# Kernel optimization log

Measured on AMD Instinct MI355X. Metric: run time of the kernel, lower is better.

## Reference

```python
import jax, jax.numpy as jnp
import numpy as np
from jax import lax

BOS = 0
B, T, U = 8, 256, 64
IN, ENC_H, DEC_H, P, J, V = 80, 512, 512, 512, 512, 1024


def lstm_layer(x, Wih, Whh, b):
    """PyTorch-style LSTM layer. x: [B,T,I]; Wih: [4H,I]; Whh: [4H,H]; b: [4H]."""
    Bn = x.shape[0]
    H = Whh.shape[1]
    xp = jnp.einsum('bti,gi->btg', x, Wih) + b  # precompute input projections [B,T,4H]
    h0 = jnp.zeros((Bn, H), x.dtype)

    def step(carry, xt):
        h, c = carry
        g = xt + h @ Whh.T
        i, f, gg, o = jnp.split(g, 4, axis=-1)
        c = jax.nn.sigmoid(f) * c + jax.nn.sigmoid(i) * jnp.tanh(gg)
        h = jax.nn.sigmoid(o) * jnp.tanh(c)
        return (h, c), h

    _, hs = lax.scan(step, (h0, h0), xp.transpose(1, 0, 2))
    return hs.transpose(1, 0, 2)  # [B,T,H]


def setup_inputs() -> dict:
    key = jax.random.key(0)
    ks = jax.random.split(key, 20)
    s = 0.04  # ~1/sqrt(H) init scale
    inp = {
        'xs': jax.random.normal(ks[0], (B, T, IN), jnp.float32),
        'ys': jax.random.randint(ks[1], (B, U), 0, V),
        # encoder LSTM layer 0 / 1
        'enc_Wih0': jax.random.normal(ks[2], (4 * ENC_H, IN), jnp.float32) * s,
        'enc_Whh0': jax.random.normal(ks[3], (4 * ENC_H, ENC_H), jnp.float32) * s,
        'enc_b0': jnp.zeros((4 * ENC_H,), jnp.float32),
        'enc_Wih1': jax.random.normal(ks[4], (4 * ENC_H, ENC_H), jnp.float32) * s,
        'enc_Whh1': jax.random.normal(ks[5], (4 * ENC_H, ENC_H), jnp.float32) * s,
        'enc_b1': jnp.zeros((4 * ENC_H,), jnp.float32),
        'enc_projW': jax.random.normal(ks[6], (P, ENC_H), jnp.float32) * s,
        'enc_projb': jnp.zeros((P,), jnp.float32),
        # decoder
        'embed': jax.random.normal(ks[7], (V, DEC_H), jnp.float32) * s,
        'dec_Wih': jax.random.normal(ks[8], (4 * DEC_H, DEC_H), jnp.float32) * s,
        'dec_Whh': jax.random.normal(ks[9], (4 * DEC_H, DEC_H), jnp.float32) * s,
        'dec_b': jnp.zeros((4 * DEC_H,), jnp.float32),
        'dec_projW': jax.random.normal(ks[10], (P, DEC_H), jnp.float32) * s,
        'dec_projb': jnp.zeros((P,), jnp.float32),
        # joint MLP: Linear(2P -> J), Tanh, Linear(J -> V)
        'jW1': jax.random.normal(ks[11], (J, 2 * P), jnp.float32) * s,
        'jb1': jnp.zeros((J,), jnp.float32),
        'jW2': jax.random.normal(ks[12], (V, J), jnp.float32) * s,
        'jb2': jnp.zeros((V,), jnp.float32),
    }
    return inp


def reference(xs, ys, enc_Wih0, enc_Whh0, enc_b0, enc_Wih1, enc_Whh1, enc_b1,
              enc_projW, enc_projb, embed, dec_Wih, dec_Whh, dec_b,
              dec_projW, dec_projb, jW1, jb1, jW2, jb2):
    # Encoder: 2-layer LSTM + projection
    h = lstm_layer(xs, enc_Wih0, enc_Whh0, enc_b0)
    h = lstm_layer(h, enc_Wih1, enc_Whh1, enc_b1)
    h_enc = h @ enc_projW.T + enc_projb  # [B,T,P]

    # Decoder: BOS pad, embed, 1-layer LSTM + projection
    ys_p = jnp.pad(ys, ((0, 0), (1, 0)), constant_values=BOS)  # [B,U+1]
    e = embed[ys_p]
    hd = lstm_layer(e, dec_Wih, dec_Whh, dec_b)
    h_dec = hd @ dec_projW.T + dec_projb  # [B,U+1,P]

    # Joint: cat([h_enc,h_dec]) @ W1.T == h_enc @ W1[:,:P].T + h_dec @ W1[:,P:].T
    pre_enc = jnp.einsum('btp,jp->btj', h_enc, jW1[:, :P])
    pre_dec = jnp.einsum('bup,jp->buj', h_dec, jW1[:, P:])
    z = jnp.tanh(pre_enc[:, :, None, :] + pre_dec[:, None, :, :] + jb1)  # [B,T,U+1,J]
    logits = jnp.einsum('btuj,vj->btuv', z, jW2) + jb2  # [B,T,U+1,V]
    return logits
```

## Files before the change

kernel.cpp:

```cpp
#include <hip/hip_runtime.h>


typedef _Float16 f16;
typedef _Float16 f16x8 __attribute__((ext_vector_type(8)));
typedef float f32x4 __attribute__((ext_vector_type(4)));
using u32 = unsigned int;

#define BB   8
#define TT   256
#define UU1  65
#define HH   512
#define G4   2048
#define PP   512
#define JJ   512
#define VV   1024
#define SENT 0xFFFFFFFFu

#define LOADX(p)     __hip_atomic_load((p), __ATOMIC_RELAXED, __HIP_MEMORY_SCOPE_AGENT)
#define STOREX(p, v) __hip_atomic_store((p), (v), __ATOMIC_RELAXED, __HIP_MEMORY_SCOPE_AGENT)

static __device__ __forceinline__ u32 packf16(float a, float b) {
  f16 ha = (f16)a, hb = (f16)b;
  unsigned short ua = __builtin_bit_cast(unsigned short, ha);
  unsigned short ub = __builtin_bit_cast(unsigned short, hb);
  return (u32)ua | ((u32)ub << 16);
}
static __device__ __forceinline__ float sigm(float x) {
  x = fminf(30.f, fmaxf(-30.f, x));
  return __builtin_amdgcn_rcpf(1.f + __expf(-x));
}
static __device__ __forceinline__ float ftanh(float x) {
  x = fminf(15.f, fmaxf(-15.f, x));
  float t = __expf(2.f * x);
  return (t - 1.f) * __builtin_amdgcn_rcpf(t + 1.f);
}

__global__ void k_init(u32* __restrict__ p, int n, int z1, int z2) {
  int i = blockIdx.x * 256 + threadIdx.x;
  if (i >= n) return;
  bool z = (i < 2048) | ((u32)(i - z1) < 2048u) | ((u32)(i - z2) < 2048u);
  p[i] = z ? 0u : SENT;
}

struct CastSeg { const float* s; f16* d; int n4; };
struct CastArgs { CastSeg seg[10]; };
__global__ void k_cast_all(CastArgs a, int total4) {
  int i = blockIdx.x * 256 + threadIdx.x;
  if (i >= total4) return;
  int k = 0, off = i;
  while (off >= a.seg[k].n4) { off -= a.seg[k].n4; ++k; }
  const float4 v = *(const float4*)(a.seg[k].s + (size_t)off * 4);
  uint2 p; p.x = packf16(v.x, v.y); p.y = packf16(v.z, v.w);
  *(uint2*)(a.seg[k].d + (size_t)off * 4) = p;
}

__global__ void k_embed(const int* __restrict__ ys, const float* __restrict__ emb,
                        float* __restrict__ e) {
  int row = blockIdx.x;
  int b = row / UU1, u = row % UU1;
  int idx = (u == 0) ? 0 : ys[b * (UU1 - 1) + (u - 1)];
  const float4* s = (const float4*)(emb + (size_t)idx * HH);
  float4* d = (float4*)(e + (size_t)row * HH);
  d[threadIdx.x] = s[threadIdx.x];
}

__global__ void k_biasdot(const float* __restrict__ jW1, const float* __restrict__ encPb,
                          const float* __restrict__ dPb, const float* __restrict__ jb1,
                          float* __restrict__ bce, float* __restrict__ bcd) {
  int j = blockIdx.x * 256 + threadIdx.x;
  if (j >= 512) return;
  const float* rowE = jW1 + (size_t)j * 1024;
  const float* rowD = rowE + 512;
  float s1 = 0.f, s2 = 0.f;
  for (int p = 0; p < 512; p += 4) {
    float4 a = *(const float4*)(rowE + p), b = *(const float4*)(encPb + p);
    s1 += a.x * b.x + a.y * b.y + a.z * b.z + a.w * b.w;
    float4 c = *(const float4*)(rowD + p), d = *(const float4*)(dPb + p);
    s2 += c.x * d.x + c.y * d.y + c.z * d.z + c.w * d.w;
  }
  bce[j] = s1; bcd[j] = s2 + jb1[j];
}

__global__ __launch_bounds__(256) void k_gemm(
    const float* __restrict__ A, const f16* __restrict__ B,
    const float* __restrict__ bias, float* __restrict__ C,
    int M, int N, int K, int lda, int ldb) {
  __shared__ f16 As[128][72];
  __shared__ f16 Bs[128][72];
  int tid = threadIdx.x;
  int mb = blockIdx.y * 128, nb = blockIdx.x * 128;
  int wave = tid >> 6, lane = tid & 63;
  int wm = wave >> 1, wn = wave & 1;
  int rowa = lane & 15, kg = lane >> 4;
  f32x4 acc[4][4] = {};
  for (int k0 = 0; k0 < K; k0 += 64) {
    for (int idx = tid; idx < 2048; idx += 256) {
      int r = idx >> 4, cq = idx & 15;
      int gm = mb + r, gk = k0 + cq * 4;
      float4 v = make_float4(0.f, 0.f, 0.f, 0.f);
      if (gm < M && gk + 3 < K) v = *(const float4*)(A + (size_t)gm * lda + gk);
      uint2 p; p.x = packf16(v.x, v.y); p.y = packf16(v.z, v.w);
      *(uint2*)&As[r][cq * 4] = p;
    }
    for (int idx = tid; idx < 1024; idx += 256) {
      int r = idx >> 3, c8 = idx & 7;
      int gn = nb + r, gk = k0 + c8 * 8;
      uint4 v = make_uint4(0u, 0u, 0u, 0u);
      if (gn < N && gk + 7 < K) v = *(const uint4*)(B + (size_t)gn * ldb + gk);
      *(uint4*)&Bs[r][c8 * 8] = v;
    }
    __syncthreads();
#pragma unroll
    for (int kf = 0; kf < 2; ++kf) {
      f16x8 af[4], bf[4];
#pragma unroll
      for (int mt = 0; mt < 4; ++mt)
        af[mt] = *(const f16x8*)&As[wm * 64 + mt * 16 + rowa][kf * 32 + kg * 8];
#pragma unroll
      for (int nt = 0; nt < 4; ++nt)
        bf[nt] = *(const f16x8*)&Bs[wn * 64 + nt * 16 + rowa][kf * 32 + kg * 8];
#pragma unroll
      for (int mt = 0; mt < 4; ++mt)
#pragma unroll
        for (int nt = 0; nt < 4; ++nt)
          acc[mt][nt] = __builtin_amdgcn_mfma_f32_16x16x32_f16(af[mt], bf[nt], acc[mt][nt], 0, 0, 0);
    }
    __syncthreads();
  }
#pragma unroll
  for (int nt = 0; nt < 4; ++nt) {
    int gn = nb + wn * 64 + nt * 16 + rowa;
    float bv = bias ? bias[gn] : 0.f;
#pragma unroll
    for (int mt = 0; mt < 4; ++mt)
#pragma unroll
      for (int r = 0; r < 4; ++r) {
        int gm = mb + wm * 64 + mt * 16 + kg * 4 + r;
        if (gm < M) C[(size_t)gm * N + gn] = acc[mt][nt][r] + bv;
      }
  }
}

__global__ __launch_bounds__(256) void k_gemmT(
    const float* __restrict__ A, int lda, const f16* __restrict__ B2,
    f16* __restrict__ C16) {
  __shared__ f16 As[128][72];
  __shared__ f16 Bs[128][72];
  int tid = threadIdx.x;
  int mb = blockIdx.y * 128, nb = blockIdx.x * 128;
  int wave = tid >> 6, lane = tid & 63;
  int wm = wave >> 1, wn = wave & 1;
  int rowa = lane & 15, kg = lane >> 4;
  f32x4 acc[4][4] = {};
  for (int k0 = 0; k0 < 512; k0 += 64) {
    for (int idx = tid; idx < 2048; idx += 256) {
      int r = idx >> 4, cq = idx & 15;
      float4 v = *(const float4*)(A + (size_t)(mb + r) * lda + k0 + cq * 4);
      uint2 p; p.x = packf16(v.x, v.y); p.y = packf16(v.z, v.w);
      *(uint2*)&As[r][cq * 4] = p;
    }
    for (int idx = tid; idx < 1024; idx += 256) {
      int r = idx >> 4, c8 = idx & 15;
      uint4 v = *(const uint4*)(B2 + (size_t)(k0 + r) * 512 + nb + c8 * 8);
      f16 tmp[8]; *(uint4*)tmp = v;
#pragma unroll
      for (int e = 0; e < 8; ++e) Bs[c8 * 8 + e][r] = tmp[e];
    }
    __syncthreads();
#pragma unroll
    for (int kf = 0; kf < 2; ++kf) {
      f16x8 af[4], bf[4];
#pragma unroll
      for (int mt = 0; mt < 4; ++mt)
        af[mt] = *(const f16x8*)&As[wm * 64 + mt * 16 + rowa][kf * 32 + kg * 8];
#pragma unroll
      for (int nt = 0; nt < 4; ++nt)
        bf[nt] = *(const f16x8*)&Bs[wn * 64 + nt * 16 + rowa][kf * 32 + kg * 8];
#pragma unroll
      for (int mt = 0; mt < 4; ++mt)
#pragma unroll
        for (int nt = 0; nt < 4; ++nt)
          acc[mt][nt] = __builtin_amdgcn_mfma_f32_16x16x32_f16(af[mt], bf[nt], acc[mt][nt], 0, 0, 0);
    }
    __syncthreads();
  }
#pragma unroll
  for (int nt = 0; nt < 4; ++nt) {
    int gn = nb + wn * 64 + nt * 16 + rowa;
#pragma unroll
    for (int mt = 0; mt < 4; ++mt)
#pragma unroll
      for (int r = 0; r < 4; ++r) {
        int gm = mb + wm * 64 + mt * 16 + kg * 4 + r;
        C16[(size_t)gm * 512 + gn] = (f16)acc[mt][nt][r];
      }
  }
}

template <int NW>
static __device__ __forceinline__ void poll_batch(const u32* const* p, u32* vv) {
#pragma unroll
  for (int k = 0; k < NW; ++k) vv[k] = LOADX(p[k]);
  int gd = 0;
  while (++gd < (1 << 18)) {
    bool any = false;
#pragma unroll
    for (int k = 0; k < NW; ++k) any = any | (vv[k] == SENT);
    if (!any) break;
    __builtin_amdgcn_s_sleep(4);
#pragma unroll
    for (int k = 0; k < NW; ++k)
      if (vv[k] == SENT) vv[k] = LOADX(p[k]);
  }
}
static __device__ __forceinline__ void guard_spin(const u32* gp) {
  u32 v = LOADX(gp);
  int gd = 0;
  while (v == SENT && ++gd < (1 << 18)) {
    __builtin_amdgcn_s_sleep(2);
    v = LOADX(gp);
  }
}

static __device__ __forceinline__ void lstm_16(
    int wg, const float* __restrict__ xp, const f16* __restrict__ Whh,
    u32* __restrict__ hseq,
    float* __restrict__ hs, int S) {
  extern __shared__ char smem[];
  f16 (*W)[520] = (f16(*)[520])smem;
  f16 (*H)[520] = (f16(*)[520])(smem + 133120);
  float (*gat)[8][36] = (float(*)[8][36])(smem + 133120 + 8320);
  const int tid = threadIdx.x;
  const int u0 = wg * 32;
  const int wave = tid >> 6, lane = tid & 63;
  const int rowa = lane & 15, kg = lane >> 4;
  const int b = lane >> 3, ju = lane & 7;
  const int uglob = u0 + wave * 8 + ju;

  for (int idx = tid; idx < 128 * 64; idx += 256) {
    int r = idx >> 6, ck = idx & 63;
    int w = r >> 5, g = (r >> 3) & 3, u = r & 7;
    uint4 v = *(const uint4*)(Whh + ((size_t)(g * 512 + u0 + w * 8 + u)) * 512 + ck * 8);
    *(uint4*)&W[r][ck * 8] = v;
  }
  __syncthreads();

  float c = 0.f;
  for (int t = 0; t < S; ++t) {
    const u32* hb = hseq + (size_t)t * 2048;
    if (tid < 16) guard_spin(hb + tid * 16);
    __syncthreads();

    size_t xpo = ((size_t)b * S + t) * (size_t)G4 + uglob;
    float xi = xp[xpo], xf = xp[xpo + 512], xg = xp[xpo + 1024], xo = xp[xpo + 1536];

    const u32* ptr[8];
    u32 vv[8];
#pragma unroll
    for (int k = 0; k < 8; ++k) ptr[k] = hb + ((tid + k * 256) >> 8) * 256 + ((tid + k * 256) & 255);
    poll_batch<8>(ptr, vv);
#pragma unroll
    for (int k = 0; k < 8; ++k) {
      int idx = tid + k * 256;
      ((u32*)H)[(idx >> 8) * 260 + (idx & 255)] = vv[k];
    }
    __syncthreads();

    f32x4 acc0 = {0.f, 0.f, 0.f, 0.f}, acc1 = {0.f, 0.f, 0.f, 0.f};
#pragma unroll
    for (int kf = 0; kf < 16; ++kf) {
      f16x8 af = {};
      if (rowa < 8) af = *(const f16x8*)&H[rowa][kf * 32 + kg * 8];
      f16x8 b0 = *(const f16x8*)&W[wave * 32 + rowa][kf * 32 + kg * 8];
      f16x8 b1 = *(const f16x8*)&W[wave * 32 + 16 + rowa][kf * 32 + kg * 8];
      acc0 = __builtin_amdgcn_mfma_f32_16x16x32_f16(af, b0, acc0, 0, 0, 0);
      acc1 = __builtin_amdgcn_mfma_f32_16x16x32_f16(af, b1, acc1, 0, 0, 0);
    }
    if (kg < 2) {
#pragma unroll
      for (int r = 0; r < 4; ++r) {
        gat[wave][kg * 4 + r][rowa] = acc0[r];
        gat[wave][kg * 4 + r][16 + rowa] = acc1[r];
      }
    }
    float gi = gat[wave][b][ju] + xi;
    float gf = gat[wave][b][8 + ju] + xf;
    float gg = gat[wave][b][16 + ju] + xg;
    float go = gat[wave][b][24 + ju] + xo;
    c = sigm(gf) * c + sigm(gi) * ftanh(gg);
    float h = sigm(go) * ftanh(c);

    float hn = __shfl_down(h, 1);
    if ((ju & 1) == 0)
      STOREX(hseq + (size_t)(t + 1) * 2048 + ((b * 512 + uglob) >> 1), packf16(h, hn));
    if (hs) hs[((size_t)b * S + t) * HH + uglob] = h;
  }
}

static __device__ __forceinline__ void lstm_l1(
    int wg, const float* __restrict__ gb, const f16* __restrict__ Wih,
    const f16* __restrict__ Whh, const u32* __restrict__ hin,
    u32* __restrict__ hseq, float* __restrict__ hs, int S) {
  extern __shared__ char smem[];
  f16 (*W)[1032] = (f16(*)[1032])smem;
  f16 (*H)[1032] = (f16(*)[1032])(smem + 132096);
  float (*gat)[8][20] = (float(*)[8][20])(smem + 132096 + 16512);
  const int tid = threadIdx.x;
  const int u0 = wg * 16;
  const int wave = tid >> 6, lane = tid & 63;
  const int rowa = lane & 15, kg = lane >> 4;
  const int b = lane >> 2, ju = lane & 3;
  const int uglob = u0 + wave * 4 + ju;

  for (int idx = tid; idx < 64 * 64; idx += 256) {
    int r = idx >> 6, ck = idx & 63;
    int w = r >> 4, g = (r >> 2) & 3, u = r & 3;
    size_t grow = (size_t)(g * 512 + u0 + w * 4 + u) * 512;
    *(uint4*)&W[r][ck * 8]       = *(const uint4*)(Whh + grow + ck * 8);
    *(uint4*)&W[r][512 + ck * 8] = *(const uint4*)(Wih + grow + ck * 8);
  }
  float gbi = 0.f, gbf = 0.f, gbg = 0.f, gbo = 0.f;
  if (lane < 32) {
    gbi = gb[uglob]; gbf = gb[512 + uglob];
    gbg = gb[1024 + uglob]; gbo = gb[1536 + uglob];
  }
  __syncthreads();

  float c = 0.f;
  for (int t = 0; t < S; ++t) {
    const u32* hbS = hseq + (size_t)t * 2048;
    const u32* hbU = hin + (size_t)(t + 1) * 2048;

    if (tid < 16) guard_spin(hbU + tid * 16);
    __syncthreads();
    {
      const u32* ptr[8];
      u32 vv[8];
#pragma unroll
      for (int k = 0; k < 8; ++k) {
        int idx = tid + k * 256;
        ptr[k] = hbU + (idx >> 8) * 256 + (idx & 255);
      }
      poll_batch<8>(ptr, vv);
#pragma unroll
      for (int k = 0; k < 8; ++k) {
        int idx = tid + k * 256;
        ((u32*)H)[(idx >> 8) * 516 + 256 + (idx & 255)] = vv[k];
      }
    }
    __syncthreads();
    f32x4 accA = {0.f, 0.f, 0.f, 0.f}, accB = {0.f, 0.f, 0.f, 0.f};
#pragma unroll
    for (int kf = 0; kf < 8; ++kf) {
      f16x8 afA = {}, afB = {};
      if (rowa < 8) {
        afA = *(const f16x8*)&H[rowa][(16 + kf) * 32 + kg * 8];
        afB = *(const f16x8*)&H[rowa][(24 + kf) * 32 + kg * 8];
      }
      f16x8 bfA = *(const f16x8*)&W[wave * 16 + rowa][(16 + kf) * 32 + kg * 8];
      f16x8 bfB = *(const f16x8*)&W[wave * 16 + rowa][(24 + kf) * 32 + kg * 8];
      accA = __builtin_amdgcn_mfma_f32_16x16x32_f16(afA, bfA, accA, 0, 0, 0);
      accB = __builtin_amdgcn_mfma_f32_16x16x32_f16(afB, bfB, accB, 0, 0, 0);
    }

    if (tid < 32) guard_spin(hbS + tid * 8);
    __syncthreads();
    {
      const u32* ptr[8];
      u32 vv[8];
#pragma unroll
      for (int k = 0; k < 8; ++k) {
        int idx = tid + k * 256;
        ptr[k] = hbS + (idx >> 8) * 256 + (idx & 255);
      }
      poll_batch<8>(ptr, vv);
#pragma unroll
      for (int k = 0; k < 8; ++k) {
        int idx = tid + k * 256;
        ((u32*)H)[(idx >> 8) * 516 + (idx & 255)] = vv[k];
      }
    }
    __syncthreads();
#pragma unroll
    for (int kf = 0; kf < 8; ++kf) {
      f16x8 afA = {}, afB = {};
      if (rowa < 8) {
        afA = *(const f16x8*)&H[rowa][kf * 32 + kg * 8];
        afB = *(const f16x8*)&H[rowa][(8 + kf) * 32 + kg * 8];
      }
      f16x8 bfA = *(const f16x8*)&W[wave * 16 + rowa][kf * 32 + kg * 8];
      f16x8 bfB = *(const f16x8*)&W[wave * 16 + rowa][(8 + kf) * 32 + kg * 8];
      accA = __builtin_amdgcn_mfma_f32_16x16x32_f16(afA, bfA, accA, 0, 0, 0);
      accB = __builtin_amdgcn_mfma_f32_16x16x32_f16(afB, bfB, accB, 0, 0, 0);
    }
    if (kg < 2) {
#pragma unroll
      for (int r = 0; r < 4; ++r) gat[wave][kg * 4 + r][rowa] = accA[r] + accB[r];
    }
    if (lane < 32) {
      float gi = gat[wave][b][ju]      + gbi;
      float gf = gat[wave][b][4 + ju]  + gbf;
      float gg = gat[wave][b][8 + ju]  + gbg;
      float go = gat[wave][b][12 + ju] + gbo;
      c = sigm(gf) * c + sigm(gi) * ftanh(gg);
      float h = sigm(go) * ftanh(c);
      float hn = __shfl_down(h, 1);
      if ((ju & 1) == 0)
        STOREX(hseq + (size_t)(t + 1) * 2048 + (b * 256 + (uglob >> 1)), packf16(h, hn));
      hs[((size_t)b * S + t) * HH + uglob] = h;
    }
  }
}

__global__ __launch_bounds__(256, 1) void k_lstm3(
    const float* xp0, const f16* Whh0, u32* hseq0,
    const float* b1, const f16* Wih1, const f16* Whh1, u32* hseq1, float* h1s,
    const float* xpd, const f16* Whhd, u32* hseqD, float* hds) {
  int g = blockIdx.x;
  if (g < 16)      lstm_16(g, xp0, Whh0, hseq0, nullptr, TT);
  else if (g < 48) lstm_l1(g - 16, b1, Wih1, Whh1, hseq0, hseq1, h1s, TT);
  else             lstm_16(g - 48, xpd, Whhd, hseqD, hds, UU1);
}

__global__ __launch_bounds__(512) void k_joint(
    const float* __restrict__ pre_enc,
    const float* __restrict__ pre_dec,
    const f16* __restrict__ jW2,
    const float* __restrict__ jb2,
    float* __restrict__ out) {
  extern __shared__ char smem[];
  f16 (*Z)[520] = (f16(*)[520])smem;
  int tid = threadIdx.x;
  int m0 = blockIdx.x * 64;
  {
    int r = tid >> 3, q = tid & 7;
    int m = m0 + r;
    int bb = m / (TT * UU1);
    int rem = m % (TT * UU1);
    int t = rem / UU1, u = rem % UU1;
    const float* pe = pre_enc + ((size_t)bb * TT + t) * JJ + q * 64;
    const float* pd = pre_dec + ((size_t)bb * UU1 + u) * JJ + q * 64;
    for (int i = 0; i < 64; i += 8) {
      float4 e0 = *(const float4*)(pe + i);
      float4 e1 = *(const float4*)(pe + i + 4);
      float4 d0 = *(const float4*)(pd + i);
      float4 d1 = *(const float4*)(pd + i + 4);
      float z0 = ftanh(e0.x + d0.x), z1 = ftanh(e0.y + d0.y);
      float z2 = ftanh(e0.z + d0.z), z3 = ftanh(e0.w + d0.w);
      float z4 = ftanh(e1.x + d1.x), z5 = ftanh(e1.y + d1.y);
      float z6 = ftanh(e1.z + d1.z), z7 = ftanh(e1.w + d1.w);
      uint4 p; p.x = packf16(z0, z1); p.y = packf16(z2, z3);
      p.z = packf16(z4, z5); p.w = packf16(z6, z7);
      *(uint4*)&Z[r][q * 64 + i] = p;
    }
  }
  __syncthreads();
  int wave = tid >> 6, lane = tid & 63;
  int wm = wave >> 2, wn = wave & 3;
  int rowa = lane & 15, kg = lane >> 4;
  for (int ch = 0; ch < 4; ++ch) {
    f32x4 acc[4][2] = {};
    int nb = ch * 256 + wn * 64;
    const f16* wb = jW2 + (size_t)(nb + rowa) * JJ + kg * 8;
    f16x8 afe[4], afo[4];
#pragma unroll
    for (int nt = 0; nt < 4; ++nt)
      afe[nt] = *(const f16x8*)(wb + (size_t)nt * 16 * JJ);
#pragma unroll
    for (int kp = 0; kp < 8; ++kp) {
      const int kfe = kp * 2, kfo = kp * 2 + 1;
#pragma unroll
      for (int nt = 0; nt < 4; ++nt)
        afo[nt] = *(const f16x8*)(wb + (size_t)nt * 16 * JJ + kfo * 32);
      {
        f16x8 bf0 = *(const f16x8*)&Z[wm * 32 + rowa][kfe * 32 + kg * 8];
        f16x8 bf1 = *(const f16x8*)&Z[wm * 32 + 16 + rowa][kfe * 32 + kg * 8];
#pragma unroll
        for (int nt = 0; nt < 4; ++nt) {
          acc[nt][0] = __builtin_amdgcn_mfma_f32_16x16x32_f16(afe[nt], bf0, acc[nt][0], 0, 0, 0);
          acc[nt][1] = __builtin_amdgcn_mfma_f32_16x16x32_f16(afe[nt], bf1, acc[nt][1], 0, 0, 0);
        }
      }
      if (kp < 7) {
#pragma unroll
        for (int nt = 0; nt < 4; ++nt)
          afe[nt] = *(const f16x8*)(wb + (size_t)nt * 16 * JJ + (kfe + 2) * 32);
      }
      {
        f16x8 bf0 = *(const f16x8*)&Z[wm * 32 + rowa][kfo * 32 + kg * 8];
        f16x8 bf1 = *(const f16x8*)&Z[wm * 32 + 16 + rowa][kfo * 32 + kg * 8];
#pragma unroll
        for (int nt = 0; nt < 4; ++nt) {
          acc[nt][0] = __builtin_amdgcn_mfma_f32_16x16x32_f16(afo[nt], bf0, acc[nt][0], 0, 0, 0);
          acc[nt][1] = __builtin_amdgcn_mfma_f32_16x16x32_f16(afo[nt], bf1, acc[nt][1], 0, 0, 0);
        }
      }
    }
#pragma unroll
    for (int nt = 0; nt < 4; ++nt) {
      int v = nb + nt * 16 + kg * 4;
      float4 bv = *(const float4*)(jb2 + v);
#pragma unroll
      for (int mt = 0; mt < 2; ++mt) {
        int m = m0 + wm * 32 + mt * 16 + rowa;
        f32x4 st;
        st[0] = acc[nt][mt][0] + bv.x;
        st[1] = acc[nt][mt][1] + bv.y;
        st[2] = acc[nt][mt][2] + bv.z;
        st[3] = acc[nt][mt][3] + bv.w;
        __builtin_nontemporal_store(st, (f32x4*)(out + (size_t)m * VV + v));
      }
    }
  }
}

extern "C" void kernel_launch(void* const* d_in, const int* in_sizes, int n_in,
                              void* d_out, int out_size, void* d_ws, size_t ws_size,
                              hipStream_t stream) {
  const float* xs    = (const float*)d_in[0];
  const int*   ys    = (const int*)d_in[1];
  const float* Wih0  = (const float*)d_in[2];
  const float* Whh0  = (const float*)d_in[3];
  const float* b0    = (const float*)d_in[4];
  const float* Wih1  = (const float*)d_in[5];
  const float* Whh1  = (const float*)d_in[6];
  const float* b1    = (const float*)d_in[7];
  const float* encPW = (const float*)d_in[8];
  const float* encPb = (const float*)d_in[9];
  const float* embed = (const float*)d_in[10];
  const float* dWih  = (const float*)d_in[11];
  const float* dWhh  = (const float*)d_in[12];
  const float* db    = (const float*)d_in[13];
  const float* dPW   = (const float*)d_in[14];
  const float* dPb   = (const float*)d_in[15];
  const float* jW1   = (const float*)d_in[16];
  const float* jb1   = (const float*)d_in[17];
  const float* jW2   = (const float*)d_in[18];
  const float* jb2   = (const float*)d_in[19];
  float* out = (float*)d_out;

  char* base = (char*)d_ws;
  size_t off = 0;
  auto alc = [&](size_t bytes) -> char* {
    char* p = base + off;
    off = (off + bytes + 255) & ~(size_t)255;
    return p;
  };
  f16* Wih0h = (f16*)alc((size_t)2048 * 80 * 2);
  f16* Whh0h = (f16*)alc((size_t)2048 * 512 * 2);
  f16* Wih1h = (f16*)alc((size_t)2048 * 512 * 2);
  f16* Whh1h = (f16*)alc((size_t)2048 * 512 * 2);
  f16* dWihh = (f16*)alc((size_t)2048 * 512 * 2);
  f16* dWhhh = (f16*)alc((size_t)2048 * 512 * 2);
  f16* ePWh  = (f16*)alc((size_t)512 * 512 * 2);
  f16* dPWh  = (f16*)alc((size_t)512 * 512 * 2);
  f16* jW2h  = (f16*)alc((size_t)1024 * 512 * 2);
  f16* Wceh  = (f16*)alc((size_t)512 * 512 * 2);
  f16* Wcdh  = (f16*)alc((size_t)512 * 512 * 2);
  float* bce  = (float*)alc((size_t)512 * 4);
  float* bcd  = (float*)alc((size_t)512 * 4);
  float* e    = (float*)alc((size_t)520 * 512 * 4);
  float* xp0  = (float*)alc((size_t)2048 * 2048 * 4);
  float* xpd  = (float*)alc((size_t)520 * 2048 * 4);
  float* h1s  = (float*)alc((size_t)2048 * 512 * 4);
  float* hds  = (float*)alc((size_t)520 * 512 * 4);
  float* penc = (float*)alc((size_t)2048 * 512 * 4);
  float* pdec = (float*)alc((size_t)520 * 512 * 4);
  u32* hseq0 = (u32*)alc((size_t)(TT + 1) * 2048 * 4);
  u32* hseq1 = (u32*)alc((size_t)(TT + 1) * 2048 * 4);
  u32* hseqD = (u32*)alc((size_t)(UU1 + 1) * 2048 * 4);
  if (off > ws_size) return;

  {
    int n = (int)(((TT + 1) * 2 + (UU1 + 1)) * 2048);
    int z1 = (int)(hseq1 - hseq0), z2 = (int)(hseqD - hseq0);
    k_init<<<dim3((n + 255) / 256), dim3(256), 0, stream>>>(hseq0, n, z1, z2);
  }
  {
    CastArgs ca = {};
    auto seg = [&](int i, const float* s, f16* d, size_t n) {
      ca.seg[i].s = s; ca.seg[i].d = d; ca.seg[i].n4 = (int)(n / 4);
    };
    seg(0, Wih0, Wih0h, (size_t)2048 * 80);
    seg(1, Whh0, Whh0h, (size_t)2048 * 512);
    seg(2, Wih1, Wih1h, (size_t)2048 * 512);
    seg(3, Whh1, Whh1h, (size_t)2048 * 512);
    seg(4, dWih, dWihh, (size_t)2048 * 512);
    seg(5, dWhh, dWhhh, (size_t)2048 * 512);
    seg(6, encPW, ePWh, (size_t)512 * 512);
    seg(7, dPW, dPWh, (size_t)512 * 512);
    seg(8, jW2, jW2h, (size_t)1024 * 512);
    int total4 = 0;
    for (int i = 0; i < 9; ++i) total4 += ca.seg[i].n4;
    k_cast_all<<<dim3((total4 + 255) / 256), dim3(256), 0, stream>>>(ca, total4);
  }
  k_gemmT<<<dim3(4, 4), dim3(256), 0, stream>>>(jW1, 1024, ePWh, Wceh);
  k_gemmT<<<dim3(4, 4), dim3(256), 0, stream>>>(jW1 + 512, 1024, dPWh, Wcdh);
  k_biasdot<<<dim3(2), dim3(256), 0, stream>>>(jW1, encPb, dPb, jb1, bce, bcd);

  k_embed<<<dim3(520), dim3(128), 0, stream>>>(ys, embed, e);

  auto gemm = [&](const float* A, const f16* B, const float* bias, float* C,
                  int M, int N, int K, int lda, int ldb) {
    k_gemm<<<dim3(N / 128, (M + 127) / 128), dim3(256), 0, stream>>>(
        A, B, bias, C, M, N, K, lda, ldb);
  };

  gemm(xs, Wih0h, b0, xp0, 2048, 2048, 80, 80, 80);
  gemm(e, dWihh, db, xpd, 520, 2048, 512, 512, 512);

  k_lstm3<<<dim3(64), dim3(256), 151168, stream>>>(
      xp0, Whh0h, hseq0,
      b1, Wih1h, Whh1h, hseq1, h1s,
      xpd, dWhhh, hseqD, hds);

  gemm(h1s, Wceh, bce, penc, 2048, 512, 512, 512, 512);
  gemm(hds, Wcdh, bcd, pdec, 520, 512, 512, 512, 512);

  k_joint<<<dim3(2080), dim3(512), 66560, stream>>>(penc, pdec, jW2h, jb2, out);
}
```

Measured before the change: 1.658 ms.

## Stage jW2 tiles in shared memory with double buffering and merge LSTM-layer-1 polls

The joint kernel now processes 128 rows per block instead of 64. It streams jW2 through a double-buffered LDS tile of 64x64 instead of loading weight fragments straight from global memory into registers. This halves the grid and reuses each weight tile across more rows, but it adds two barriers per iteration and needs about 148KB of LDS, which limits occupancy to one block per CU. Separately, the layer-1 LSTM step now waits for both its own previous hidden state and the layer-0 input together, then runs one merged MFMA loop, which removes a barrier phase but loses the overlap between the input part and the recurrent wait.

New measurement: 1.485 ms. -10.4%, faster.

```diff
diff --git a/kernel.cpp b/kernel.cpp
--- a/kernel.cpp
+++ b/kernel.cpp
@@ -330,66 +330,38 @@
   for (int t = 0; t < S; ++t) {
     const u32* hbS = hseq + (size_t)t * 2048;
     const u32* hbU = hin + (size_t)(t + 1) * 2048;
-
-    if (tid < 16) guard_spin(hbU + tid * 16);
-    __syncthreads();
-    {
-      const u32* ptr[8];
-      u32 vv[8];
-#pragma unroll
-      for (int k = 0; k < 8; ++k) {
-        int idx = tid + k * 256;
-        ptr[k] = hbU + (idx >> 8) * 256 + (idx & 255);
-      }
-      poll_batch<8>(ptr, vv);
-#pragma unroll
-      for (int k = 0; k < 8; ++k) {
-        int idx = tid + k * 256;
-        ((u32*)H)[(idx >> 8) * 516 + 256 + (idx & 255)] = vv[k];
-      }
-    }
-    __syncthreads();
+    if (tid < 32)       guard_spin(hbS + tid * 8);
+    else if (tid < 48)  guard_spin(hbU + (tid - 32) * 16);
+    __syncthreads();
+    const u32* ptr[16];
+    u32 vv[16];
+#pragma unroll
+    for (int k = 0; k < 8; ++k) {
+      int idx = tid + k * 256;
+      int r = idx >> 8, cu = idx & 255;
+      ptr[k] = hbS + r * 256 + cu;
+      ptr[k + 8] = hbU + r * 256 + cu;
+    }
+    poll_batch<16>(ptr, vv);
+#pragma unroll
+    for (int k = 0; k < 8; ++k) {
+      int idx = tid + k * 256;
+      int r = idx >> 8, cu = idx & 255;
+      ((u32*)H)[r * 516 + cu] = vv[k];
+      ((u32*)H)[r * 516 + 256 + cu] = vv[k + 8];
+    }
+    __syncthreads();
+
     f32x4 accA = {0.f, 0.f, 0.f, 0.f}, accB = {0.f, 0.f, 0.f, 0.f};
 #pragma unroll
-    for (int kf = 0; kf < 8; ++kf) {
-      f16x8 afA = {}, afB = {};
-      if (rowa < 8) {
-        afA = *(const f16x8*)&H[rowa][(16 + kf) * 32 + kg * 8];
-        afB = *(const f16x8*)&H[rowa][(24 + kf) * 32 + kg * 8];
-      }
-      f16x8 bfA = *(const f16x8*)&W[wave * 16 + rowa][(16 + kf) * 32 + kg * 8];
-      f16x8 bfB = *(const f16x8*)&W[wave * 16 + rowa][(24 + kf) * 32 + kg * 8];
-      accA = __builtin_amdgcn_mfma_f32_16x16x32_f16(afA, bfA, accA, 0, 0, 0);
-      accB = __builtin_amdgcn_mfma_f32_16x16x32_f16(afB, bfB, accB, 0, 0, 0);
-    }
-
-    if (tid < 32) guard_spin(hbS + tid * 8);
-    __syncthreads();
-    {
-      const u32* ptr[8];
-      u32 vv[8];
-#pragma unroll
-      for (int k = 0; k < 8; ++k) {
-        int idx = tid + k * 256;
-        ptr[k] = hbS + (idx >> 8) * 256 + (idx & 255);
-      }
-      poll_batch<8>(ptr, vv);
-#pragma unroll
-      for (int k = 0; k < 8; ++k) {
-        int idx = tid + k * 256;
-        ((u32*)H)[(idx >> 8) * 516 + (idx & 255)] = vv[k];
-      }
-    }
-    __syncthreads();
-#pragma unroll
-    for (int kf = 0; kf < 8; ++kf) {
+    for (int kf = 0; kf < 16; ++kf) {
       f16x8 afA = {}, afB = {};
       if (rowa < 8) {
         afA = *(const f16x8*)&H[rowa][kf * 32 + kg * 8];
-        afB = *(const f16x8*)&H[rowa][(8 + kf) * 32 + kg * 8];
+        afB = *(const f16x8*)&H[rowa][(kf + 16) * 32 + kg * 8];
       }
       f16x8 bfA = *(const f16x8*)&W[wave * 16 + rowa][kf * 32 + kg * 8];
-      f16x8 bfB = *(const f16x8*)&W[wave * 16 + rowa][(8 + kf) * 32 + kg * 8];
+      f16x8 bfB = *(const f16x8*)&W[wave * 16 + rowa][(kf + 16) * 32 + kg * 8];
       accA = __builtin_amdgcn_mfma_f32_16x16x32_f16(afA, bfA, accA, 0, 0, 0);
       accB = __builtin_amdgcn_mfma_f32_16x16x32_f16(afB, bfB, accB, 0, 0, 0);
     }
@@ -430,17 +402,18 @@
     float* __restrict__ out) {
   extern __shared__ char smem[];
   f16 (*Z)[520] = (f16(*)[520])smem;
+  f16 (*Bs)[64][72] = (f16(*)[64][72])(smem + 133120);
   int tid = threadIdx.x;
-  int m0 = blockIdx.x * 64;
+  int m0 = blockIdx.x * 128;
   {
-    int r = tid >> 3, q = tid & 7;
+    int r = tid >> 2, q = tid & 3;
     int m = m0 + r;
     int bb = m / (TT * UU1);
     int rem = m % (TT * UU1);
     int t = rem / UU1, u = rem % UU1;
-    const float* pe = pre_enc + ((size_t)bb * TT + t) * JJ + q * 64;
-    const float* pd = pre_dec + ((size_t)bb * UU1 + u) * JJ + q * 64;
-    for (int i = 0; i < 64; i += 8) {
+    const float* pe = pre_enc + ((size_t)bb * TT + t) * JJ + q * 128;
+    const float* pd = pre_dec + ((size_t)bb * UU1 + u) * JJ + q * 128;
+    for (int i = 0; i < 128; i += 8) {
       float4 e0 = *(const float4*)(pe + i);
       float4 e1 = *(const float4*)(pe + i + 4);
       float4 d0 = *(const float4*)(pd + i);
@@ -451,66 +424,63 @@
       float z6 = ftanh(e1.z + d1.z), z7 = ftanh(e1.w + d1.w);
       uint4 p; p.x = packf16(z0, z1); p.y = packf16(z2, z3);
       p.z = packf16(z4, z5); p.w = packf16(z6, z7);
-      *(uint4*)&Z[r][q * 64 + i] = p;
-    }
+      *(uint4*)&Z[r][q * 128 + i] = p;
+    }
+  }
+  const int wave = tid >> 6, lane = tid & 63;
+  const int wm = wave >> 1, wn = wave & 1;
+  const int rowa = lane & 15, kg = lane >> 4;
+  const int r8 = tid >> 3, c8 = tid & 7;
+
+  {
+    uint4 v = *(const uint4*)(jW2 + (size_t)r8 * JJ + c8 * 8);
+    *(uint4*)&Bs[0][r8][c8 * 8] = v;
   }
   __syncthreads();
-  int wave = tid >> 6, lane = tid & 63;
-  int wm = wave >> 2, wn = wave & 3;
-  int rowa = lane & 15, kg = lane >> 4;
-  for (int ch = 0; ch < 4; ++ch) {
-    f32x4 acc[4][2] = {};
-    int nb = ch * 256 + wn * 64;
-    const f16* wb = jW2 + (size_t)(nb + rowa) * JJ + kg * 8;
-    f16x8 afe[4], afo[4];
-#pragma unroll
-    for (int nt = 0; nt < 4; ++nt)
-      afe[nt] = *(const f16x8*)(wb + (size_t)nt * 16 * JJ);
-#pragma unroll
-    for (int kp = 0; kp < 8; ++kp) {
-      const int kfe = kp * 2, kfo = kp * 2 + 1;
-#pragma unroll
-      for (int nt = 0; nt < 4; ++nt)
-        afo[nt] = *(const f16x8*)(wb + (size_t)nt * 16 * JJ + kfo * 32);
-      {
-        f16x8 bf0 = *(const f16x8*)&Z[wm * 32 + rowa][kfe * 32 + kg * 8];
-        f16x8 bf1 = *(const f16x8*)&Z[wm * 32 + 16 + rowa][kfe * 32 + kg * 8];
-#pragma unroll
-        for (int nt = 0; nt < 4; ++nt) {
-          acc[nt][0] = __builtin_amdgcn_mfma_f32_16x16x32_f16(afe[nt], bf0, acc[nt][0], 0, 0, 0);
-          acc[nt][1] = __builtin_amdgcn_mfma_f32_16x16x32_f16(afe[nt], bf1, acc[nt][1], 0, 0, 0);
+
+  f32x4 acc[2][2] = {};
+  for (int it = 0; it < 128; ++it) {
+    const int buf = it & 1;
+    uint4 nreg;
+    if (it < 127) {
+      int nvc = (it + 1) >> 3, nks = (it + 1) & 7;
+      nreg = *(const uint4*)(jW2 + (size_t)(nvc * 64 + r8) * JJ + nks * 64 + c8 * 8);
+    }
+    const int ks = it & 7;
+#pragma unroll
+    for (int kf = 0; kf < 2; ++kf) {
+      int zo = ks * 64 + kf * 32 + kg * 8;
+      f16x8 af0 = *(const f16x8*)&Bs[buf][wn * 32 + rowa][kf * 32 + kg * 8];
+      f16x8 af1 = *(const f16x8*)&Bs[buf][wn * 32 + 16 + rowa][kf * 32 + kg * 8];
+      f16x8 bf0 = *(const f16x8*)&Z[wm * 32 + rowa][zo];
+      f16x8 bf1 = *(const f16x8*)&Z[wm * 32 + 16 + rowa][zo];
+      acc[0][0] = __builtin_amdgcn_mfma_f32_16x16x32_f16(af0, bf0, acc[0][0], 0, 0, 0);
+      acc[0][1] = __builtin_amdgcn_mfma_f32_16x16x32_f16(af0, bf1, acc[0][1], 0, 0, 0);
+      acc[1][0] = __builtin_amdgcn_mfma_f32_16x16x32_f16(af1, bf0, acc[1][0], 0, 0, 0);
+      acc[1][1] = __builtin_amdgcn_mfma_f32_16x16x32_f16(af1, bf1, acc[1][1], 0, 0, 0);
+    }
+    if (ks == 7) {
+      int vc = it >> 3;
+#pragma unroll
+      for (int nt = 0; nt < 2; ++nt) {
+        int v = vc * 64 + wn * 32 + nt * 16 + kg * 4;
+        float4 bv = *(const float4*)(jb2 + v);
+#pragma unroll
+        for (int mt = 0; mt < 2; ++mt) {
+          int m = m0 + wm * 32 + mt * 16 + rowa;
+          f32x4 st;
+          st[0] = acc[nt][mt][0] + bv.x;
+          st[1] = acc[nt][mt][1] + bv.y;
+          st[2] = acc[nt][mt][2] + bv.z;
+          st[3] = acc[nt][mt][3] + bv.w;
+          __builtin_nontemporal_store(st, (f32x4*)(out + (size_t)m * VV + v));
+          acc[nt][mt] = (f32x4){0.f, 0.f, 0.f, 0.f};
         }
       }
-      if (kp < 7) {
-#pragma unroll
-        for (int nt = 0; nt < 4; ++nt)
-          afe[nt] = *(const f16x8*)(wb + (size_t)nt * 16 * JJ + (kfe + 2) * 32);
-      }
-      {
-        f16x8 bf0 = *(const f16x8*)&Z[wm * 32 + rowa][kfo * 32 + kg * 8];
-        f16x8 bf1 = *(const f16x8*)&Z[wm * 32 + 16 + rowa][kfo * 32 + kg * 8];
-#pragma unroll
-        for (int nt = 0; nt < 4; ++nt) {
-          acc[nt][0] = __builtin_amdgcn_mfma_f32_16x16x32_f16(afo[nt], bf0, acc[nt][0], 0, 0, 0);
-          acc[nt][1] = __builtin_amdgcn_mfma_f32_16x16x32_f16(afo[nt], bf1, acc[nt][1], 0, 0, 0);
-        }
-      }
-    }
-#pragma unroll
-    for (int nt = 0; nt < 4; ++nt) {
-      int v = nb + nt * 16 + kg * 4;
-      float4 bv = *(const float4*)(jb2 + v);
-#pragma unroll
-      for (int mt = 0; mt < 2; ++mt) {
-        int m = m0 + wm * 32 + mt * 16 + rowa;
-        f32x4 st;
-        st[0] = acc[nt][mt][0] + bv.x;
-        st[1] = acc[nt][mt][1] + bv.y;
-        st[2] = acc[nt][mt][2] + bv.z;
-        st[3] = acc[nt][mt][3] + bv.w;
-        __builtin_nontemporal_store(st, (f32x4*)(out + (size_t)m * VV + v));
-      }
-    }
+    }
+    __syncthreads();
+    if (it < 127) *(uint4*)&Bs[buf ^ 1][r8][c8 * 8] = nreg;
+    __syncthreads();
   }
 }
 
@@ -617,5 +587,5 @@
   gemm(h1s, Wceh, bce, penc, 2048, 512, 512, 512, 512);
   gemm(hds, Wcdh, bcd, pdec, 520, 512, 512, 512, 512);
 
-  k_joint<<<dim3(2080), dim3(512), 66560, stream>>>(penc, pdec, jW2h, jb2, out);
-}
+  k_joint<<<dim3(1040), dim3(512), 151552, stream>>>(penc, pdec, jW2h, jb2, out);
+}
```
